# Optimization experiments

Measured on AMD Instinct MI355X. Metric: run time of the kernel, lower is better.

Reference implementation:

```python
import jax, jax.numpy as jnp
import numpy as np

B, C, CI, H, W = 4, 64, 32, 96, 96  # batch, in_channels, inter_channels, spatial
EPS = 1e-5


def conv1x1(x, w, b):
    # x: [B,Cin,H,W], w: [Cout,Cin], b: [Cout]
    return jnp.einsum('bchw,oc->bohw', x, w) + b[None, :, None, None]


def maxpool2(x):
    b, c, h, w = x.shape
    return x.reshape(b, c, h // 2, 2, w // 2, 2).max(axis=(3, 5))


def setup_inputs() -> dict:
    key = jax.random.key(0)
    ks = jax.random.split(key, 12)
    s = 0.05  # keep unscaled attention logits in a sane range
    return {
        'x': jax.random.normal(ks[0], (B, C, H, W), jnp.float32),
        'feature': jax.random.normal(ks[1], (B, CI, H, W), jnp.float32),
        'g_w': jax.random.normal(ks[2], (C, C), jnp.float32) * s,
        'g_b': jax.random.normal(ks[3], (C,), jnp.float32) * s,
        'theta_w': jax.random.normal(ks[4], (C, C), jnp.float32) * s,
        'theta_b': jax.random.normal(ks[5], (C,), jnp.float32) * s,
        'phi_w': jax.random.normal(ks[6], (C, CI), jnp.float32) * s,
        'phi_b': jax.random.normal(ks[7], (C,), jnp.float32) * s,
        'W_w': jax.random.normal(ks[8], (CI, C), jnp.float32) * s,
        'W_b': jax.random.normal(ks[9], (CI,), jnp.float32) * s,
        'bn_gamma': jax.random.normal(ks[10], (CI,), jnp.float32) * s + 1.0,
        'bn_beta': jax.random.normal(ks[11], (CI,), jnp.float32) * s,
    }


def reference(x, feature, g_w, g_b, theta_w, theta_b, phi_w, phi_b, W_w, W_b, bn_gamma, bn_beta):
    b = x.shape[0]
    # g branch: conv1x1 then 2x2 maxpool -> [B, M, C]
    g_x = maxpool2(conv1x1(x, g_w, g_b)).reshape(b, C, -1).transpose(0, 2, 1)
    # theta: conv1x1 -> [B, N, C]
    theta_x = conv1x1(x, theta_w, theta_b).reshape(b, C, -1).transpose(0, 2, 1)
    # phi on `feature` (inter_channels -> in_channels) then maxpool -> [B, C, M]
    phi_f = maxpool2(conv1x1(feature, phi_w, phi_b)).reshape(b, C, -1)
    # unscaled attention: [B, N, M]
    f = jnp.einsum('bnc,bcm->bnm', theta_x, phi_f)
    f_div_C = jax.nn.softmax(f, axis=-1)
    y = jnp.einsum('bnm,bmc->bnc', f_div_C, g_x)  # [B, N, C]
    y = y.transpose(0, 2, 1).reshape(x.shape)
    z = y + x
    # W: conv1x1 (C -> CI) + BatchNorm2d (training mode, batch stats)
    z = conv1x1(z, W_w, W_b)
    mean = z.mean(axis=(0, 2, 3), keepdims=True)
    var = z.var(axis=(0, 2, 3), keepdims=True)
    z = (z - mean) * jax.lax.rsqrt(var + EPS)
    z = z * bn_gamma[None, :, None, None] + bn_beta[None, :, None, None]
    return z
```

## Files before the change

kernel.cpp:

```cpp
#include <hip/hip_runtime.h>
#include <hip/hip_bf16.h>

typedef __attribute__((ext_vector_type(8))) short short8;
typedef __attribute__((ext_vector_type(4))) float f32x4;

#define NB 4
#define NN 9216
#define NM 2304
#define MSPLIT 4
#define MSL (NM / MSPLIT)

__device__ inline unsigned pk2(float a, float b) {
  __hip_bfloat16 ha = __float2bfloat16(a), hb = __float2bfloat16(b);
  return (unsigned)*(unsigned short*)&ha | ((unsigned)*(unsigned short*)&hb << 16);
}
__device__ inline float b2f(short s) {
  unsigned u = ((unsigned)(unsigned short)s) << 16; return *(float*)&u;
}
__device__ inline short8 pack8(const float* v) {
  short8 s;
#pragma unroll
  for (int j = 0; j < 8; ++j) { __hip_bfloat16 h = __float2bfloat16(v[j]); s[j] = *(short*)&h; }
  return s;
}
__device__ inline short8 ldw8(const float* p) {
  float tmp[8];
  *(float4*)&tmp[0] = *(const float4*)p;
  *(float4*)&tmp[4] = *(const float4*)(p + 4);
  return pack8(tmp);
}

__global__ __launch_bounds__(256) void conv_pool_k(
    const float* __restrict__ x, const float* __restrict__ feat,
    const float* __restrict__ tw, const float* __restrict__ tbi,
    const float* __restrict__ gw, const float* __restrict__ gbi,
    const float* __restrict__ pw, const float* __restrict__ pbi,
    __hip_bfloat16* __restrict__ Theta, __hip_bfloat16* __restrict__ Gcm,
    __hip_bfloat16* __restrict__ PhiT, float* __restrict__ psum) {
  int t = threadIdx.x, wv = t >> 6, lane = t & 63, l15 = lane & 15, q = lane >> 4;
  int b = blockIdx.y, bx = blockIdx.x;
  if (bx == 0 && b == 0 && t < 64) psum[t] = 0.f;
  int jt = bx % 6, rp = bx / 6;
  int i0 = rp * 2, j0 = jt * 16;
  int ntop = i0 * 96 + j0;
  int ot = wv;

  short8 wt[2], wg[2], wp1;
#pragma unroll
  for (int kf = 0; kf < 2; ++kf) {
    wt[kf] = ldw8(tw + (size_t)(ot * 16 + l15) * 64 + kf * 32 + q * 8);
    wg[kf] = ldw8(gw + (size_t)(ot * 16 + l15) * 64 + kf * 32 + q * 8);
  }
  wp1 = ldw8(pw + (size_t)(ot * 16 + l15) * 32 + q * 8);

  short8 bxf[2][2], bff[2];
  {
    float tmp[8];
#pragma unroll
    for (int row = 0; row < 2; ++row) {
#pragma unroll
      for (int kf = 0; kf < 2; ++kf) {
#pragma unroll
        for (int j = 0; j < 8; ++j)
          tmp[j] = x[((size_t)b * 64 + kf * 32 + q * 8 + j) * NN + ntop + row * 96 + l15];
        bxf[row][kf] = pack8(tmp);
      }
#pragma unroll
      for (int j = 0; j < 8; ++j)
        tmp[j] = feat[((size_t)b * 32 + q * 8 + j) * NN + ntop + row * 96 + l15];
      bff[row] = pack8(tmp);
    }
  }

  int m = rp * 48 + ((j0 + l15) >> 1);
  bool em = (l15 & 1) == 0;

#pragma unroll
  for (int row = 0; row < 2; ++row) {
    f32x4 d;
#pragma unroll
    for (int r = 0; r < 4; ++r) d[r] = tbi[ot * 16 + q * 4 + r];
    d = __builtin_amdgcn_mfma_f32_16x16x32_bf16(wt[0], bxf[row][0], d, 0, 0, 0);
    d = __builtin_amdgcn_mfma_f32_16x16x32_bf16(wt[1], bxf[row][1], d, 0, 0, 0);
    size_t base = ((size_t)b * NN + ntop + row * 96 + l15) * 64 + ot * 16 + q * 4;
    *(unsigned*)(Theta + base) = pk2(d[0], d[1]);
    *(unsigned*)(Theta + base + 2) = pk2(d[2], d[3]);
  }
  {
    f32x4 d0, d1;
#pragma unroll
    for (int r = 0; r < 4; ++r) { float bb = gbi[ot * 16 + q * 4 + r]; d0[r] = bb; d1[r] = bb; }
    d0 = __builtin_amdgcn_mfma_f32_16x16x32_bf16(wg[0], bxf[0][0], d0, 0, 0, 0);
    d0 = __builtin_amdgcn_mfma_f32_16x16x32_bf16(wg[1], bxf[0][1], d0, 0, 0, 0);
    d1 = __builtin_amdgcn_mfma_f32_16x16x32_bf16(wg[0], bxf[1][0], d1, 0, 0, 0);
    d1 = __builtin_amdgcn_mfma_f32_16x16x32_bf16(wg[1], bxf[1][1], d1, 0, 0, 0);
    float h[4];
#pragma unroll
    for (int r = 0; r < 4; ++r) {
      float v = fmaxf(d0[r], d1[r]);
      h[r] = fmaxf(v, __shfl_xor(v, 1));
    }
    if (em) {
#pragma unroll
      for (int r = 0; r < 4; ++r)
        Gcm[((size_t)b * 64 + ot * 16 + q * 4 + r) * NM + m] = __float2bfloat16(h[r]);
    }
  }
  {
    f32x4 d0, d1;
#pragma unroll
    for (int r = 0; r < 4; ++r) { float bb = pbi[ot * 16 + q * 4 + r]; d0[r] = bb; d1[r] = bb; }
    d0 = __builtin_amdgcn_mfma_f32_16x16x32_bf16(wp1, bff[0], d0, 0, 0, 0);
    d1 = __builtin_amdgcn_mfma_f32_16x16x32_bf16(wp1, bff[1], d1, 0, 0, 0);
    float h[4];
#pragma unroll
    for (int r = 0; r < 4; ++r) {
      float v = fmaxf(d0[r], d1[r]);
      h[r] = fmaxf(v, __shfl_xor(v, 1));
    }
    if (em) {
      size_t base = ((size_t)b * NM + m) * 64 + ot * 16 + q * 4;
      *(unsigned*)(PhiT + base) = pk2(h[0], h[1]);
      *(unsigned*)(PhiT + base + 2) = pk2(h[2], h[3]);
    }
  }
}

__global__ __launch_bounds__(256) void attn_part(
    const __hip_bfloat16* __restrict__ Theta, const __hip_bfloat16* __restrict__ PhiT,
    const __hip_bfloat16* __restrict__ Gcm,
    __hip_bfloat16* __restrict__ ypart, float* __restrict__ rsumpart) {
  __shared__ __align__(16) __hip_bfloat16 phis[32][72];
  __shared__ __align__(16) __hip_bfloat16 gs[64][40];
  __shared__ __align__(16) __hip_bfloat16 pbuf[4][16][40];

  int t = threadIdx.x, wv = t >> 6, lane = t & 63;
  int l15 = lane & 15, q = lane >> 4;
  int bx = blockIdx.x;
  int nb = bx % 144, split = bx / 144;
  int b = blockIdx.y;
  int n0 = nb * 64, nw = n0 + wv * 16;
  int mbase = split * MSL;

  const __hip_bfloat16* trow = Theta + ((size_t)b * NN + nw + l15) * 64 + q * 8;
  short8 ta0 = *(const short8*)trow;
  short8 ta1 = *(const short8*)(trow + 32);

  f32x4 acc[4];
#pragma unroll
  for (int ct = 0; ct < 4; ++ct) acc[ct] = (f32x4){0.f, 0.f, 0.f, 0.f};
  float rsum[4] = {0.f, 0.f, 0.f, 0.f};

  const __hip_bfloat16* phibase = PhiT + (size_t)b * NM * 64;
  const __hip_bfloat16* gbase = Gcm + (size_t)b * 64 * NM;

  for (int ck = 0; ck < MSL / 32; ++ck) {
    int m0 = mbase + ck * 32;
    __syncthreads();
    {
      int r = t >> 3, seg = t & 7;
      *(uint4*)&phis[r][seg * 8] = *(const uint4*)(phibase + (size_t)(m0 + r) * 64 + seg * 8);
    }
    {
      int r = t >> 2, seg = t & 3;
      *(uint4*)&gs[r][seg * 8] = *(const uint4*)(gbase + (size_t)r * NM + m0 + seg * 8);
    }
    __syncthreads();

#pragma unroll
    for (int tm = 0; tm < 2; ++tm) {
      short8 pb0 = *(const short8*)&phis[tm * 16 + l15][q * 8];
      short8 pb1 = *(const short8*)&phis[tm * 16 + l15][32 + q * 8];
      f32x4 s = (f32x4){0.f, 0.f, 0.f, 0.f};
      s = __builtin_amdgcn_mfma_f32_16x16x32_bf16(ta0, pb0, s, 0, 0, 0);
      s = __builtin_amdgcn_mfma_f32_16x16x32_bf16(ta1, pb1, s, 0, 0, 0);
#pragma unroll
      for (int r = 0; r < 4; ++r) {
        float e = __expf(s[r]);
        rsum[r] += e;
        pbuf[wv][q * 4 + r][tm * 16 + l15] = __float2bfloat16(e);
      }
    }
    short8 pa = *(const short8*)&pbuf[wv][l15][q * 8];
#pragma unroll
    for (int ct = 0; ct < 4; ++ct) {
      short8 gb = *(const short8*)&gs[ct * 16 + l15][q * 8];
      acc[ct] = __builtin_amdgcn_mfma_f32_16x16x32_bf16(pa, gb, acc[ct], 0, 0, 0);
    }
  }

#pragma unroll
  for (int r = 0; r < 4; ++r) {
    float v = rsum[r];
    v += __shfl_xor(v, 1); v += __shfl_xor(v, 2);
    v += __shfl_xor(v, 4); v += __shfl_xor(v, 8);
    if (l15 == 0)
      rsumpart[(size_t)(split * NB + b) * NN + nw + q * 4 + r] = v;
  }
#pragma unroll
  for (int ct = 0; ct < 4; ++ct)
#pragma unroll
    for (int r = 0; r < 4; ++r)
      ypart[((size_t)(split * NB + b) * NN + nw + q * 4 + r) * 64 + ct * 16 + l15] =
          __float2bfloat16(acc[ct][r]);
}

__global__ __launch_bounds__(256) void combine_k(
    const __hip_bfloat16* __restrict__ ypart, const float* __restrict__ rsumpart,
    const float* __restrict__ x, const float* __restrict__ Ww, const float* __restrict__ Wb,
    float* __restrict__ z2, float* __restrict__ psum) {
  __shared__ float rs[4][64];
  int t = threadIdx.x, wv = t >> 6, lane = t & 63;
  int l15 = lane & 15, q = lane >> 4;
  int b = blockIdx.y, n0 = blockIdx.x * 64, nw = n0 + wv * 16;
  int nrow = nw + l15;

  float y0[8], y1[8];
#pragma unroll
  for (int j = 0; j < 8; ++j) { y0[j] = 0.f; y1[j] = 0.f; }
  float rsum = 0.f;
#pragma unroll
  for (int s = 0; s < MSPLIT; ++s) {
    const __hip_bfloat16* yp = ypart + ((size_t)(s * NB + b) * NN + nrow) * 64;
    short8 a = *(const short8*)(yp + q * 8);
    short8 c = *(const short8*)(yp + 32 + q * 8);
#pragma unroll
    for (int j = 0; j < 8; ++j) { y0[j] += b2f(a[j]); y1[j] += b2f(c[j]); }
    rsum += rsumpart[(size_t)(s * NB + b) * NN + nrow];
  }
  float rinv = 1.0f / rsum;

  float z1a[8], z1b[8];
#pragma unroll
  for (int j = 0; j < 8; ++j) {
    z1a[j] = y0[j] * rinv + x[((size_t)b * 64 + q * 8 + j) * NN + nrow];
    z1b[j] = y1[j] * rinv + x[((size_t)b * 64 + 32 + q * 8 + j) * NN + nrow];
  }
  short8 za0 = pack8(z1a), za1 = pack8(z1b);

  short8 wbf[2][2];
#pragma unroll
  for (int ot = 0; ot < 2; ++ot)
#pragma unroll
    for (int kf = 0; kf < 2; ++kf)
      wbf[ot][kf] = ldw8(Ww + (size_t)(ot * 16 + l15) * 64 + kf * 32 + q * 8);

  f32x4 dd[2];
#pragma unroll
  for (int ot = 0; ot < 2; ++ot) {
    float bias = Wb[ot * 16 + l15];
    f32x4 d = (f32x4){bias, bias, bias, bias};
    d = __builtin_amdgcn_mfma_f32_16x16x32_bf16(za0, wbf[ot][0], d, 0, 0, 0);
    d = __builtin_amdgcn_mfma_f32_16x16x32_bf16(za1, wbf[ot][1], d, 0, 0, 0);
#pragma unroll
    for (int r = 0; r < 4; ++r)
      z2[((size_t)b * NN + nw + q * 4 + r) * 32 + ot * 16 + l15] = d[r];
    dd[ot] = d;
  }

#pragma unroll
  for (int ot = 0; ot < 2; ++ot) {
    float ps = (dd[ot][0] + dd[ot][1]) + (dd[ot][2] + dd[ot][3]);
    float ps2 = dd[ot][0] * dd[ot][0] + dd[ot][1] * dd[ot][1] +
                dd[ot][2] * dd[ot][2] + dd[ot][3] * dd[ot][3];
    ps += __shfl_xor(ps, 16);  ps += __shfl_xor(ps, 32);
    ps2 += __shfl_xor(ps2, 16); ps2 += __shfl_xor(ps2, 32);
    if (lane < 16) {
      rs[wv][ot * 16 + lane] = ps;
      rs[wv][32 + ot * 16 + lane] = ps2;
    }
  }
  __syncthreads();
  if (t < 64) {
    float tot = rs[0][t] + rs[1][t] + rs[2][t] + rs[3][t];
    atomicAdd(&psum[t], tot);
  }
}

__global__ __launch_bounds__(256) void bn_apply(
    const float* __restrict__ z2, const float* __restrict__ psum,
    const float* __restrict__ gamma, const float* __restrict__ beta,
    float* __restrict__ out) {
  __shared__ float ssl[64];
  __shared__ float zt[32][65];
  int t = threadIdx.x, b = blockIdx.y, n0 = blockIdx.x * 64;
  if (t < 32) {
    const float inv = 1.0f / (float)(NB * NN);
    float mean = psum[t] * inv;
    float var = psum[32 + t] * inv - mean * mean;
    float sc = gamma[t] * rsqrtf(var + 1e-5f);
    ssl[t] = sc;
    ssl[32 + t] = beta[t] - mean * sc;
  }
#pragma unroll
  for (int it = 0; it < 2; ++it) {
    int idx = it * 256 + t, r = idx >> 3, seg = idx & 7;
    float4 vv = *(const float4*)(z2 + ((size_t)b * NN + n0 + r) * 32 + seg * 4);
    zt[seg * 4 + 0][r] = vv.x; zt[seg * 4 + 1][r] = vv.y;
    zt[seg * 4 + 2][r] = vv.z; zt[seg * 4 + 3][r] = vv.w;
  }
  __syncthreads();
  int o = t >> 3, nseg = t & 7;
  float sc = ssl[o], sh = ssl[32 + o];
  float4 a, c;
  a.x = zt[o][nseg * 8 + 0] * sc + sh; a.y = zt[o][nseg * 8 + 1] * sc + sh;
  a.z = zt[o][nseg * 8 + 2] * sc + sh; a.w = zt[o][nseg * 8 + 3] * sc + sh;
  c.x = zt[o][nseg * 8 + 4] * sc + sh; c.y = zt[o][nseg * 8 + 5] * sc + sh;
  c.z = zt[o][nseg * 8 + 6] * sc + sh; c.w = zt[o][nseg * 8 + 7] * sc + sh;
  float* po = out + ((size_t)b * 32 + o) * NN + n0 + nseg * 8;
  *(float4*)po = a;
  *(float4*)(po + 4) = c;
}

extern "C" void kernel_launch(void* const* d_in, const int* in_sizes, int n_in,
                              void* d_out, int out_size, void* d_ws, size_t ws_size,
                              hipStream_t stream) {
  const float* x       = (const float*)d_in[0];
  const float* feature = (const float*)d_in[1];
  const float* g_w     = (const float*)d_in[2];
  const float* g_b     = (const float*)d_in[3];
  const float* theta_w = (const float*)d_in[4];
  const float* theta_b = (const float*)d_in[5];
  const float* phi_w   = (const float*)d_in[6];
  const float* phi_b   = (const float*)d_in[7];
  const float* W_w     = (const float*)d_in[8];
  const float* W_b     = (const float*)d_in[9];
  const float* bn_g    = (const float*)d_in[10];
  const float* bn_b    = (const float*)d_in[11];

  char* ws = (char*)d_ws;
  __hip_bfloat16* Theta    = (__hip_bfloat16*)(ws);
  __hip_bfloat16* Gcm      = (__hip_bfloat16*)(ws + 4718592);
  __hip_bfloat16* PhiT     = (__hip_bfloat16*)(ws + 5898240);
  float*          z2       = (float*)(ws + 7077888);
  __hip_bfloat16* ypart    = (__hip_bfloat16*)(ws + 11796480);
  float*          rsumpart = (float*)(ws + 30670848);
  float*          psum     = (float*)(ws + 31260672);

  conv_pool_k<<<dim3(288, NB), dim3(256), 0, stream>>>(
      x, feature, theta_w, theta_b, g_w, g_b, phi_w, phi_b, Theta, Gcm, PhiT, psum);
  attn_part<<<dim3(144 * MSPLIT, NB), dim3(256), 0, stream>>>(
      Theta, PhiT, Gcm, ypart, rsumpart);
  combine_k<<<dim3(144, NB), dim3(256), 0, stream>>>(
      ypart, rsumpart, x, W_w, W_b, z2, psum);
  bn_apply<<<dim3(144, NB), dim3(256), 0, stream>>>(
      z2, psum, bn_g, bn_b, (float*)d_out);
}
```

Before: 165.2 us.

## Compute transposed scores so exp output feeds PV MFMA directly in fp16

The attention kernel now computes S^T (phi as A operand, theta as B), so each lane's exp values already sit in the A-operand layout of a 16x16x16 f16 MFMA. This removes the LDS round trip through pbuf. G is stored as fp16 and loaded into LDS with a matching permutation. Each wave now handles 32 query rows with 128-thread blocks, and the M split drops from 4 to 2, which halves the partial-sum traffic. The combine kernel is resized to match. fp16 exp values risk overflow only if the logits are large.

After: 173.7 us. +5.1%, slower.

```diff
diff --git a/kernel.cpp b/kernel.cpp
--- a/kernel.cpp
+++ b/kernel.cpp
@@ -3,11 +3,13 @@
 
 typedef __attribute__((ext_vector_type(8))) short short8;
 typedef __attribute__((ext_vector_type(4))) float f32x4;
+typedef __attribute__((ext_vector_type(4))) _Float16 half4;
+typedef __attribute__((ext_vector_type(8))) _Float16 half8;
 
 #define NB 4
 #define NN 9216
 #define NM 2304
-#define MSPLIT 4
+#define MSPLIT 2
 #define MSL (NM / MSPLIT)
 
 __device__ inline unsigned pk2(float a, float b) {
@@ -35,7 +37,7 @@
     const float* __restrict__ tw, const float* __restrict__ tbi,
     const float* __restrict__ gw, const float* __restrict__ gbi,
     const float* __restrict__ pw, const float* __restrict__ pbi,
-    __hip_bfloat16* __restrict__ Theta, __hip_bfloat16* __restrict__ Gcm,
+    __hip_bfloat16* __restrict__ Theta, _Float16* __restrict__ Gcm,
     __hip_bfloat16* __restrict__ PhiT, float* __restrict__ psum) {
   int t = threadIdx.x, wv = t >> 6, lane = t & 63, l15 = lane & 15, q = lane >> 4;
   int b = blockIdx.y, bx = blockIdx.x;
@@ -103,7 +105,7 @@
     if (em) {
 #pragma unroll
       for (int r = 0; r < 4; ++r)
-        Gcm[((size_t)b * 64 + ot * 16 + q * 4 + r) * NM + m] = __float2bfloat16(h[r]);
+        Gcm[((size_t)b * 64 + ot * 16 + q * 4 + r) * NM + m] = (_Float16)h[r];
     }
   }
   {
@@ -126,93 +128,119 @@
   }
 }
 
-__global__ __launch_bounds__(256) void attn_part(
+__global__ __launch_bounds__(128) void attn_part(
     const __hip_bfloat16* __restrict__ Theta, const __hip_bfloat16* __restrict__ PhiT,
-    const __hip_bfloat16* __restrict__ Gcm,
+    const _Float16* __restrict__ Gcm,
     __hip_bfloat16* __restrict__ ypart, float* __restrict__ rsumpart) {
   __shared__ __align__(16) __hip_bfloat16 phis[32][72];
-  __shared__ __align__(16) __hip_bfloat16 gs[64][40];
-  __shared__ __align__(16) __hip_bfloat16 pbuf[4][16][40];
+  __shared__ __align__(16) _Float16 gs2[64][40];
 
   int t = threadIdx.x, wv = t >> 6, lane = t & 63;
   int l15 = lane & 15, q = lane >> 4;
   int bx = blockIdx.x;
   int nb = bx % 144, split = bx / 144;
   int b = blockIdx.y;
-  int n0 = nb * 64, nw = n0 + wv * 16;
+  int n0 = nb * 64, nw = n0 + wv * 32;
   int mbase = split * MSL;
 
-  const __hip_bfloat16* trow = Theta + ((size_t)b * NN + nw + l15) * 64 + q * 8;
-  short8 ta0 = *(const short8*)trow;
-  short8 ta1 = *(const short8*)(trow + 32);
-
-  f32x4 acc[4];
-#pragma unroll
-  for (int ct = 0; ct < 4; ++ct) acc[ct] = (f32x4){0.f, 0.f, 0.f, 0.f};
-  float rsum[4] = {0.f, 0.f, 0.f, 0.f};
+  short8 tb[2][2];
+#pragma unroll
+  for (int nt = 0; nt < 2; ++nt)
+#pragma unroll
+    for (int kf = 0; kf < 2; ++kf)
+      tb[nt][kf] = *(const short8*)(Theta + ((size_t)b * NN + nw + nt * 16 + l15) * 64 + kf * 32 + q * 8);
+
+  f32x4 acc[2][4];
+#pragma unroll
+  for (int nt = 0; nt < 2; ++nt)
+#pragma unroll
+    for (int ct = 0; ct < 4; ++ct) acc[nt][ct] = (f32x4){0.f, 0.f, 0.f, 0.f};
+  float rsum[2] = {0.f, 0.f};
 
   const __hip_bfloat16* phibase = PhiT + (size_t)b * NM * 64;
-  const __hip_bfloat16* gbase = Gcm + (size_t)b * 64 * NM;
+  const _Float16* gbase = Gcm + (size_t)b * 64 * NM;
 
   for (int ck = 0; ck < MSL / 32; ++ck) {
     int m0 = mbase + ck * 32;
     __syncthreads();
-    {
-      int r = t >> 3, seg = t & 7;
+#pragma unroll
+    for (int p = 0; p < 2; ++p) {
+      int idx = p * 128 + t, r = idx >> 3, seg = idx & 7;
       *(uint4*)&phis[r][seg * 8] = *(const uint4*)(phibase + (size_t)(m0 + r) * 64 + seg * 8);
     }
-    {
-      int r = t >> 2, seg = t & 3;
-      *(uint4*)&gs[r][seg * 8] = *(const uint4*)(gbase + (size_t)r * NM + m0 + seg * 8);
+#pragma unroll
+    for (int p = 0; p < 2; ++p) {
+      int idx = p * 128 + t, c = idx >> 2, qq = idx & 3;
+      const _Float16* gc = gbase + (size_t)c * NM + m0 + qq * 4;
+      uint2 lo = *(const uint2*)gc;
+      uint2 hi = *(const uint2*)(gc + 16);
+      uint4 w; w.x = lo.x; w.y = lo.y; w.z = hi.x; w.w = hi.y;
+      *(uint4*)&gs2[c][qq * 8] = w;
     }
     __syncthreads();
 
-#pragma unroll
-    for (int tm = 0; tm < 2; ++tm) {
-      short8 pb0 = *(const short8*)&phis[tm * 16 + l15][q * 8];
-      short8 pb1 = *(const short8*)&phis[tm * 16 + l15][32 + q * 8];
-      f32x4 s = (f32x4){0.f, 0.f, 0.f, 0.f};
-      s = __builtin_amdgcn_mfma_f32_16x16x32_bf16(ta0, pb0, s, 0, 0, 0);
-      s = __builtin_amdgcn_mfma_f32_16x16x32_bf16(ta1, pb1, s, 0, 0, 0);
-#pragma unroll
-      for (int r = 0; r < 4; ++r) {
-        float e = __expf(s[r]);
-        rsum[r] += e;
-        pbuf[wv][q * 4 + r][tm * 16 + l15] = __float2bfloat16(e);
+    short8 pha[2][2];
+#pragma unroll
+    for (int tm = 0; tm < 2; ++tm)
+#pragma unroll
+      for (int kf = 0; kf < 2; ++kf)
+        pha[tm][kf] = *(const short8*)&phis[tm * 16 + l15][kf * 32 + q * 8];
+    half8 gv[4];
+#pragma unroll
+    for (int ct = 0; ct < 4; ++ct)
+      gv[ct] = *(const half8*)&gs2[ct * 16 + l15][q * 8];
+
+#pragma unroll
+    for (int nt = 0; nt < 2; ++nt) {
+      f32x4 s0 = (f32x4){0.f, 0.f, 0.f, 0.f};
+      s0 = __builtin_amdgcn_mfma_f32_16x16x32_bf16(pha[0][0], tb[nt][0], s0, 0, 0, 0);
+      s0 = __builtin_amdgcn_mfma_f32_16x16x32_bf16(pha[0][1], tb[nt][1], s0, 0, 0, 0);
+      f32x4 s1 = (f32x4){0.f, 0.f, 0.f, 0.f};
+      s1 = __builtin_amdgcn_mfma_f32_16x16x32_bf16(pha[1][0], tb[nt][0], s1, 0, 0, 0);
+      s1 = __builtin_amdgcn_mfma_f32_16x16x32_bf16(pha[1][1], tb[nt][1], s1, 0, 0, 0);
+
+      float e0 = __expf(s0[0]), e1 = __expf(s0[1]), e2 = __expf(s0[2]), e3 = __expf(s0[3]);
+      float f0 = __expf(s1[0]), f1 = __expf(s1[1]), f2 = __expf(s1[2]), f3 = __expf(s1[3]);
+      rsum[nt] += ((e0 + e1) + (e2 + e3)) + ((f0 + f1) + (f2 + f3));
+      half4 pa0 = {(_Float16)e0, (_Float16)e1, (_Float16)e2, (_Float16)e3};
+      half4 pa1 = {(_Float16)f0, (_Float16)f1, (_Float16)f2, (_Float16)f3};
+
+#pragma unroll
+      for (int ct = 0; ct < 4; ++ct) {
+        half4 glo = __builtin_shufflevector(gv[ct], gv[ct], 0, 1, 2, 3);
+        half4 ghi = __builtin_shufflevector(gv[ct], gv[ct], 4, 5, 6, 7);
+        acc[nt][ct] = __builtin_amdgcn_mfma_f32_16x16x16f16(pa0, glo, acc[nt][ct], 0, 0, 0);
+        acc[nt][ct] = __builtin_amdgcn_mfma_f32_16x16x16f16(pa1, ghi, acc[nt][ct], 0, 0, 0);
       }
     }
-    short8 pa = *(const short8*)&pbuf[wv][l15][q * 8];
-#pragma unroll
-    for (int ct = 0; ct < 4; ++ct) {
-      short8 gb = *(const short8*)&gs[ct * 16 + l15][q * 8];
-      acc[ct] = __builtin_amdgcn_mfma_f32_16x16x32_bf16(pa, gb, acc[ct], 0, 0, 0);
-    }
-  }
-
-#pragma unroll
-  for (int r = 0; r < 4; ++r) {
-    float v = rsum[r];
-    v += __shfl_xor(v, 1); v += __shfl_xor(v, 2);
-    v += __shfl_xor(v, 4); v += __shfl_xor(v, 8);
-    if (l15 == 0)
-      rsumpart[(size_t)(split * NB + b) * NN + nw + q * 4 + r] = v;
-  }
-#pragma unroll
-  for (int ct = 0; ct < 4; ++ct)
-#pragma unroll
-    for (int r = 0; r < 4; ++r)
-      ypart[((size_t)(split * NB + b) * NN + nw + q * 4 + r) * 64 + ct * 16 + l15] =
-          __float2bfloat16(acc[ct][r]);
-}
-
-__global__ __launch_bounds__(256) void combine_k(
+  }
+
+#pragma unroll
+  for (int nt = 0; nt < 2; ++nt) {
+    float v = rsum[nt];
+    v += __shfl_xor(v, 16);
+    v += __shfl_xor(v, 32);
+    if (lane < 16)
+      rsumpart[(size_t)(split * NB + b) * NN + nw + nt * 16 + lane] = v;
+  }
+#pragma unroll
+  for (int nt = 0; nt < 2; ++nt)
+#pragma unroll
+    for (int ct = 0; ct < 4; ++ct)
+#pragma unroll
+      for (int r = 0; r < 4; ++r)
+        ypart[((size_t)(split * NB + b) * NN + nw + nt * 16 + q * 4 + r) * 64 + ct * 16 + l15] =
+            __float2bfloat16(acc[nt][ct][r]);
+}
+
+__global__ __launch_bounds__(128) void combine_k(
     const __hip_bfloat16* __restrict__ ypart, const float* __restrict__ rsumpart,
     const float* __restrict__ x, const float* __restrict__ Ww, const float* __restrict__ Wb,
     float* __restrict__ z2, float* __restrict__ psum) {
-  __shared__ float rs[4][64];
+  __shared__ float rs[2][64];
   int t = threadIdx.x, wv = t >> 6, lane = t & 63;
   int l15 = lane & 15, q = lane >> 4;
-  int b = blockIdx.y, n0 = blockIdx.x * 64, nw = n0 + wv * 16;
+  int b = blockIdx.y, n0 = blockIdx.x * 32, nw = n0 + wv * 16;
   int nrow = nw + l15;
 
   float y0[8], y1[8];
@@ -271,10 +299,7 @@
     }
   }
   __syncthreads();
-  if (t < 64) {
-    float tot = rs[0][t] + rs[1][t] + rs[2][t] + rs[3][t];
-    atomicAdd(&psum[t], tot);
-  }
+  if (t < 64) atomicAdd(&psum[t], rs[0][t] + rs[1][t]);
 }
 
 __global__ __launch_bounds__(256) void bn_apply(
@@ -330,18 +355,18 @@
 
   char* ws = (char*)d_ws;
   __hip_bfloat16* Theta    = (__hip_bfloat16*)(ws);
-  __hip_bfloat16* Gcm      = (__hip_bfloat16*)(ws + 4718592);
+  _Float16*       Gcm      = (_Float16*)(ws + 4718592);
   __hip_bfloat16* PhiT     = (__hip_bfloat16*)(ws + 5898240);
   float*          z2       = (float*)(ws + 7077888);
   __hip_bfloat16* ypart    = (__hip_bfloat16*)(ws + 11796480);
-  float*          rsumpart = (float*)(ws + 30670848);
-  float*          psum     = (float*)(ws + 31260672);
+  float*          rsumpart = (float*)(ws + 21233664);
+  float*          psum     = (float*)(ws + 21528576);
 
   conv_pool_k<<<dim3(288, NB), dim3(256), 0, stream>>>(
       x, feature, theta_w, theta_b, g_w, g_b, phi_w, phi_b, Theta, Gcm, PhiT, psum);
-  attn_part<<<dim3(144 * MSPLIT, NB), dim3(256), 0, stream>>>(
+  attn_part<<<dim3(144 * MSPLIT, NB), dim3(128), 0, stream>>>(
       Theta, PhiT, Gcm, ypart, rsumpart);
-  combine_k<<<dim3(144, NB), dim3(256), 0, stream>>>(
+  combine_k<<<dim3(288, NB), dim3(128), 0, stream>>>(
       ypart, rsumpart, x, W_w, W_b, z2, psum);
   bn_apply<<<dim3(144, NB), dim3(256), 0, stream>>>(
       z2, psum, bn_g, bn_b, (float*)d_out);
```
